# Performance work log

Hardware: AMD Instinct MI355X
Metric: run time of the kernel (lower is better)

## Reference

```python
import jax, jax.numpy as jnp
import numpy as np

NUM_HEADS = 32
HEAD_DIM = 128
HIDDEN = 4096
MAX_SEQ = 4096
B, S = 8, 16
POS = 2048


def setup_inputs() -> dict:
    key = jax.random.key(0)
    ks = jax.random.split(key, 7)
    sc = 1.0 / np.sqrt(HIDDEN)
    return {
        "h": jax.random.normal(ks[0], (B, S, HIDDEN), dtype=jnp.float32),
        "Wq": jax.random.normal(ks[1], (HIDDEN, HIDDEN), dtype=jnp.float32) * sc,
        "Wk": jax.random.normal(ks[2], (HIDDEN, HIDDEN), dtype=jnp.float32) * sc,
        "Wv": jax.random.normal(ks[3], (HIDDEN, HIDDEN), dtype=jnp.float32) * sc,
        "Wo": jax.random.normal(ks[4], (HIDDEN, HIDDEN), dtype=jnp.float32) * sc,
        "K_cache": jax.random.normal(ks[5], (B, NUM_HEADS, MAX_SEQ, HEAD_DIM), dtype=jnp.float32),
        "V_cache": jax.random.normal(ks[6], (B, NUM_HEADS, MAX_SEQ, HEAD_DIM), dtype=jnp.float32),
        "pos": POS,
    }


def reference(h, Wq, Wk, Wv, Wo, K_cache, V_cache, pos):
    b, s, _ = h.shape
    # QKV projections (Linear with weight [out, in], no bias): h @ W.T
    def proj(W):
        return (h @ W.T).reshape(b, s, NUM_HEADS, HEAD_DIM).transpose(0, 2, 1, 3)  # [B,H,S,hd]
    Q, K, V = proj(Wq), proj(Wk), proj(Wv)
    # write new K/V into cache at [pos : pos+S] (pos is a static Python int)
    K_cache = K_cache.at[:, :, pos:pos + s, :].set(K)
    V_cache = V_cache.at[:, :, pos:pos + s, :].set(V)
    K_all = K_cache[:, :, :pos + s, :]  # [B,H,T,hd], T = pos+S
    V_all = V_cache[:, :, :pos + s, :]
    scores = jnp.einsum('bhsd,bhtd->bhst', Q, K_all) / np.sqrt(HEAD_DIM)  # [B,H,S,T]
    if s > 1:
        # causal mask applied only to the freshly-written block of columns
        causal = jnp.triu(jnp.full((s, s), -jnp.inf, dtype=scores.dtype), k=1)
        scores = scores.at[:, :, :, pos:pos + s].add(causal)
    attn = jax.nn.softmax(scores, axis=-1)
    out = jnp.einsum('bhst,bhtd->bhsd', attn, V_all)  # [B,H,S,hd]
    out = out.transpose(0, 2, 1, 3).reshape(b, s, NUM_HEADS * HEAD_DIM)
    return out @ Wo.T
```

## Files before the change

kernel.cpp:

```cpp
#include <hip/hip_runtime.h>

typedef _Float16 f16;
typedef _Float16 f16x8 __attribute__((ext_vector_type(8)));
typedef _Float16 f16x2 __attribute__((ext_vector_type(2)));
typedef float f32x4 __attribute__((ext_vector_type(4)));
typedef float f32x2 __attribute__((ext_vector_type(2)));

#define MFMA16(a, b, c) __builtin_amdgcn_mfma_f32_16x16x32_f16(a, b, c, 0, 0, 0)

#define HID 4096
#define ROWS 128
#define SCL 0.12751743f

__device__ __forceinline__ f16x8 cvt8(float4 x, float4 y) {
    f16x8 v = {(f16)x.x, (f16)x.y, (f16)x.z, (f16)x.w,
               (f16)y.x, (f16)y.y, (f16)y.z, (f16)y.w};
    return v;
}

__device__ __forceinline__ int swz2(int row, int cb) {
    return row * 256 + (cb ^ ((row & 7) << 4));
}

__global__ void k_cvt(const float* __restrict__ src, f16* __restrict__ dst) {
    const int i = blockIdx.x * blockDim.x + threadIdx.x;
    const float4* s4 = (const float4*)src + (size_t)i * 2;
    float4 x = s4[0], y = s4[1];
    *((f16x8*)dst + i) = cvt8(x, y);
}

__global__ __launch_bounds__(256) void k_proj(
        const f16* __restrict__ hb,
        const float* __restrict__ Wq, const float* __restrict__ Wk,
        const float* __restrict__ Wv,
        f16* __restrict__ Qw, f16* __restrict__ Kw, f16* __restrict__ Vw) {
    const int mat = blockIdx.x >> 8;
    const int ct  = blockIdx.x & 255;
    const float* __restrict__ W = (mat == 0) ? Wq : (mat == 1) ? Wk : Wv;
    f16* __restrict__ Ob = (mat == 0) ? Qw : (mat == 1) ? Kw : Vw;
    const int c0 = ct * 16;

    __shared__ __align__(16) f16 sA[128 * 128];
    __shared__ __align__(16) f16 sB[16 * 128];

    const int tid = threadIdx.x;
    const int w = tid >> 6, l = tid & 63;
    const int rw = w * 32;
    const int ar = tid >> 4;
    const int ac = (tid & 15) * 8;

    f32x4 acc0 = {}, acc1 = {};

    for (int ks = 0; ks < 32; ++ks) {
        const int k0 = ks * 128;
        #pragma unroll
        for (int c = 0; c < 8; ++c) {
            const int row = c * 16 + ar;
            f16x8 v = *(const f16x8*)(hb + (size_t)row * HID + k0 + ac);
            *(f16x8*)((char*)sA + swz2(row, ac * 2)) = v;
        }
        {
            const float* wp = W + (size_t)(c0 + ar) * HID + k0 + ac;
            float4 x = *(const float4*)wp;
            float4 y = *(const float4*)(wp + 4);
            *(f16x8*)((char*)sB + swz2(ar, ac * 2)) = cvt8(x, y);
        }
        __syncthreads();
        #pragma unroll
        for (int kk = 0; kk < 4; ++kk) {
            const int cb = kk * 64 + (l >> 4) * 16;
            f16x8 a0 = *(const f16x8*)((char*)sA + swz2(rw + (l & 15), cb));
            f16x8 a1 = *(const f16x8*)((char*)sA + swz2(rw + 16 + (l & 15), cb));
            f16x8 b0 = *(const f16x8*)((char*)sB + swz2((l & 15), cb));
            acc0 = MFMA16(a0, b0, acc0);
            acc1 = MFMA16(a1, b0, acc1);
        }
        __syncthreads();
    }
    #pragma unroll
    for (int r = 0; r < 4; ++r) {
        const int col = c0 + (l & 15);
        Ob[(size_t)(rw + (l >> 4) * 4 + r) * HID + col]      = (f16)acc0[r];
        Ob[(size_t)(rw + 16 + (l >> 4) * 4 + r) * HID + col] = (f16)acc1[r];
    }
}

__global__ __launch_bounds__(1024) void k_attn(
        const f16* __restrict__ Qw, const f16* __restrict__ Kw,
        const f16* __restrict__ Vw,
        const float* __restrict__ Kc, const float* __restrict__ Vc,
        const int* __restrict__ posp, f16* __restrict__ Ow) {

    __shared__ __align__(16) char smem[131072 + 2048];

    const int bh = blockIdx.x;
    const int b = bh >> 5, hh = bh & 31;
    const int tid = threadIdx.x, w = tid >> 6, l = tid & 63;
    const int pos = *posp;
    const int ntiles = (pos + 16 + 31) >> 5;

    const float* Kb = Kc + (size_t)bh * (4096 * 128);
    const float* Vb = Vc + (size_t)bh * (4096 * 128);

    f16x8 qf[4];
    {
        const f16* qp = Qw + (size_t)(b * 16 + (l & 15)) * HID + hh * 128 + (l >> 4) * 8;
        #pragma unroll
        for (int kk = 0; kk < 4; ++kk) qf[kk] = *(const f16x8*)(qp + kk * 32);
    }

    f32x4 o[8] = {};
    float m[4], lsum[4];
    #pragma unroll
    for (int r = 0; r < 4; ++r) { m[r] = -3e38f; lsum[r] = 0.f; }

    f16* Pw = (f16*)smem + w * 640;

    for (int tau = w; tau < ntiles; tau += 16) {
        const int t0 = tau * 32;
        const bool pure = (t0 + 32 <= pos);
        f32x4 sa[2] = {};

        if (pure) {
            #pragma unroll
            for (int tn = 0; tn < 2; ++tn) {
                const float* kp = Kb + (size_t)(t0 + tn * 16 + (l & 15)) * 128 + (l >> 4) * 8;
                #pragma unroll
                for (int kk = 0; kk < 4; ++kk) {
                    float4 x = *(const float4*)(kp + kk * 32);
                    float4 y = *(const float4*)(kp + kk * 32 + 4);
                    sa[tn] = MFMA16(qf[kk], cvt8(x, y), sa[tn]);
                }
            }
        } else {
            #pragma unroll
            for (int tn = 0; tn < 2; ++tn) {
                const int trow = t0 + tn * 16 + (l & 15);
                f16x8 kf[4];
                if (trow < pos) {
                    const float* kp = Kb + (size_t)trow * 128 + (l >> 4) * 8;
                    #pragma unroll
                    for (int kk = 0; kk < 4; ++kk) {
                        float4 x = *(const float4*)(kp + kk * 32);
                        float4 y = *(const float4*)(kp + kk * 32 + 4);
                        kf[kk] = cvt8(x, y);
                    }
                } else {
                    const int tt = trow - pos;
                    const int rr = tt < 15 ? tt : 15;
                    const f16* kp = Kw + (size_t)(b * 16 + rr) * HID + hh * 128 + (l >> 4) * 8;
                    #pragma unroll
                    for (int kk = 0; kk < 4; ++kk) kf[kk] = *(const f16x8*)(kp + kk * 32);
                }
                #pragma unroll
                for (int kk = 0; kk < 4; ++kk) sa[tn] = MFMA16(qf[kk], kf[kk], sa[tn]);
            }
        }

        float sc[2][4];
        #pragma unroll
        for (int tn = 0; tn < 2; ++tn)
            #pragma unroll
            for (int r = 0; r < 4; ++r) sc[tn][r] = sa[tn][r] * SCL;
        if (!pure) {
            #pragma unroll
            for (int tn = 0; tn < 2; ++tn) {
                const int tg = t0 + tn * 16 + (l & 15);
                if (tg >= pos) {
                    const int tt = tg - pos;
                    #pragma unroll
                    for (int r = 0; r < 4; ++r) {
                        const int s_ = (l >> 4) * 4 + r;
                        if (tt > s_ || tt >= 16) sc[tn][r] = -3e38f;
                    }
                }
            }
        }

        float vmax[4];
        #pragma unroll
        for (int r = 0; r < 4; ++r) vmax[r] = fmaxf(sc[0][r], sc[1][r]);
        #pragma unroll
        for (int d = 1; d < 16; d <<= 1)
            #pragma unroll
            for (int r = 0; r < 4; ++r) vmax[r] = fmaxf(vmax[r], __shfl_xor(vmax[r], d));
        float p[2][4], rs[4], fac[4];
        #pragma unroll
        for (int r = 0; r < 4; ++r) {
            const float mn = fmaxf(m[r], vmax[r]);
            fac[r] = exp2f(m[r] - mn);
            m[r] = mn;
            p[0][r] = sc[0][r] < -1e29f ? 0.f : exp2f(sc[0][r] - mn);
            p[1][r] = sc[1][r] < -1e29f ? 0.f : exp2f(sc[1][r] - mn);
            rs[r] = p[0][r] + p[1][r];
            lsum[r] *= fac[r];
        }
        #pragma unroll
        for (int d = 1; d < 16; d <<= 1)
            #pragma unroll
            for (int r = 0; r < 4; ++r) rs[r] += __shfl_xor(rs[r], d);
        #pragma unroll
        for (int r = 0; r < 4; ++r) lsum[r] += rs[r];
        #pragma unroll
        for (int dt = 0; dt < 8; ++dt)
            #pragma unroll
            for (int r = 0; r < 4; ++r) o[dt][r] *= fac[r];

        #pragma unroll
        for (int r = 0; r < 4; ++r) {
            const int s_ = (l >> 4) * 4 + r;
            Pw[s_ * 40 + (l & 15)]      = (f16)p[0][r];
            Pw[s_ * 40 + 16 + (l & 15)] = (f16)p[1][r];
        }
        asm volatile("s_waitcnt lgkmcnt(0)" ::: "memory");
        f16x8 pa = *(const f16x8*)(Pw + (l & 15) * 40 + (l >> 4) * 8);

        if (pure) {
            const float* vp = Vb + (size_t)(t0 + (l >> 4) * 8) * 128 + (l & 15);
            #pragma unroll
            for (int dt = 0; dt < 8; ++dt) {
                f16x8 vf;
                #pragma unroll
                for (int j = 0; j < 8; ++j) vf[j] = (f16)vp[j * 128 + dt * 16];
                o[dt] = MFMA16(pa, vf, o[dt]);
            }
        } else {
            const int tb = t0 + (l >> 4) * 8;
            #pragma unroll
            for (int dt = 0; dt < 8; ++dt) {
                f16x8 vf;
                #pragma unroll
                for (int j = 0; j < 8; ++j) {
                    const int t = tb + j;
                    if (t < pos) {
                        vf[j] = (f16)Vb[(size_t)t * 128 + dt * 16 + (l & 15)];
                    } else {
                        const int rr = (t - pos < 15) ? (t - pos) : 15;
                        vf[j] = Vw[(size_t)(b * 16 + rr) * HID + hh * 128 + dt * 16 + (l & 15)];
                    }
                }
                o[dt] = MFMA16(pa, vf, o[dt]);
            }
        }
    }

    __syncthreads();
    float* Osh = (float*)smem;
    float* Msh = (float*)(smem + 131072);
    float* Lsh = Msh + 256;
    #pragma unroll
    for (int dt = 0; dt < 8; ++dt)
        #pragma unroll
        for (int r = 0; r < 4; ++r)
            Osh[w * 2048 + ((l >> 4) * 4 + r) * 128 + dt * 16 + (l & 15)] = o[dt][r];
    if ((l & 15) == 0) {
        #pragma unroll
        for (int r = 0; r < 4; ++r) {
            Msh[w * 16 + (l >> 4) * 4 + r] = m[r];
            Lsh[w * 16 + (l >> 4) * 4 + r] = lsum[r];
        }
    }
    __syncthreads();
    {
        const int s_ = tid >> 6;
        const int d_ = (tid & 63) * 2;
        float M = -3e38f;
        #pragma unroll
        for (int ww = 0; ww < 16; ++ww) M = fmaxf(M, Msh[ww * 16 + s_]);
        float L = 0.f, o0 = 0.f, o1 = 0.f;
        #pragma unroll
        for (int ww = 0; ww < 16; ++ww) {
            const float e = exp2f(Msh[ww * 16 + s_] - M);
            L += e * Lsh[ww * 16 + s_];
            f32x2 v = *(const f32x2*)(Osh + ww * 2048 + s_ * 128 + d_);
            o0 += e * v.x;
            o1 += e * v.y;
        }
        const float inv = 1.f / L;
        f16x2 res = {(f16)(o0 * inv), (f16)(o1 * inv)};
        *(f16x2*)(Ow + (size_t)(b * 16 + s_) * HID + hh * 128 + d_) = res;
    }
}

__global__ __launch_bounds__(256) void k_oproj(
        const f16* __restrict__ Oa, const float* __restrict__ Wo,
        float* __restrict__ out) {
    const int c0 = blockIdx.x * 16;

    __shared__ __align__(16) f16 sA[128 * 128];
    __shared__ __align__(16) f16 sB[16 * 128];

    const int tid = threadIdx.x;
    const int w = tid >> 6, l = tid & 63;
    const int rw = w * 32;
    const int ar = tid >> 4;
    const int ac = (tid & 15) * 8;

    f32x4 acc0 = {}, acc1 = {};

    for (int ks = 0; ks < 32; ++ks) {
        const int k0 = ks * 128;
        #pragma unroll
        for (int c = 0; c < 8; ++c) {
            const int row = c * 16 + ar;
            f16x8 v = *(const f16x8*)(Oa + (size_t)row * HID + k0 + ac);
            *(f16x8*)((char*)sA + swz2(row, ac * 2)) = v;
        }
        {
            const float* wp = Wo + (size_t)(c0 + ar) * HID + k0 + ac;
            float4 x = *(const float4*)wp;
            float4 y = *(const float4*)(wp + 4);
            *(f16x8*)((char*)sB + swz2(ar, ac * 2)) = cvt8(x, y);
        }
        __syncthreads();
        #pragma unroll
        for (int kk = 0; kk < 4; ++kk) {
            const int cb = kk * 64 + (l >> 4) * 16;
            f16x8 a0 = *(const f16x8*)((char*)sA + swz2(rw + (l & 15), cb));
            f16x8 a1 = *(const f16x8*)((char*)sA + swz2(rw + 16 + (l & 15), cb));
            f16x8 b0 = *(const f16x8*)((char*)sB + swz2((l & 15), cb));
            acc0 = MFMA16(a0, b0, acc0);
            acc1 = MFMA16(a1, b0, acc1);
        }
        __syncthreads();
    }
    #pragma unroll
    for (int r = 0; r < 4; ++r) {
        const int col = c0 + (l & 15);
        out[(size_t)(rw + (l >> 4) * 4 + r) * HID + col]      = acc0[r];
        out[(size_t)(rw + 16 + (l >> 4) * 4 + r) * HID + col] = acc1[r];
    }
}

extern "C" void kernel_launch(void* const* d_in, const int* in_sizes, int n_in,
                              void* d_out, int out_size, void* d_ws, size_t ws_size,
                              hipStream_t stream) {
    const float* h  = (const float*)d_in[0];
    const float* Wq = (const float*)d_in[1];
    const float* Wk = (const float*)d_in[2];
    const float* Wv = (const float*)d_in[3];
    const float* Wo = (const float*)d_in[4];
    const float* Kc = (const float*)d_in[5];
    const float* Vc = (const float*)d_in[6];
    const int* pos  = (const int*)d_in[7];
    float* out = (float*)d_out;

    f16* hws = (f16*)d_ws;
    f16* Qw  = hws + ROWS * HID;
    f16* Kw  = Qw + ROWS * HID;
    f16* Vw  = Kw + ROWS * HID;
    f16* Ow  = Vw + ROWS * HID;

    k_cvt<<<256, 256, 0, stream>>>(h, hws);
    k_proj<<<768, 256, 0, stream>>>(hws, Wq, Wk, Wv, Qw, Kw, Vw);
    k_attn<<<256, 1024, 0, stream>>>(Qw, Kw, Vw, Kc, Vc, pos, Ow);
    k_oproj<<<256, 256, 0, stream>>>(Ow, Wo, out);
}
```

Baseline: 241.3 us.

## Register-prefetch GEMM tiles and restructure attention into contiguous per-wave tile ranges

Both projection GEMMs now load the next K-slice of activations and weights into registers while the current slice is multiplied, so global loads overlap with MFMA work. The attention kernel drops from 16 to 8 waves per block. Each wave now processes a contiguous range of unmasked KV tiles with no masking branches, and V loads are issued earlier. A single wave handles the tail tiles that touch the new tokens, and the final reduction across waves uses wider vectors. This adds register pressure and a possible load imbalance from the tail wave, but cuts branching and lets more latency overlap.

```diff
diff --git a/kernel.cpp b/kernel.cpp
--- a/kernel.cpp
+++ b/kernel.cpp
@@ -2,6 +2,7 @@
 
 typedef _Float16 f16;
 typedef _Float16 f16x8 __attribute__((ext_vector_type(8)));
+typedef _Float16 f16x4 __attribute__((ext_vector_type(4)));
 typedef _Float16 f16x2 __attribute__((ext_vector_type(2)));
 typedef float f32x4 __attribute__((ext_vector_type(4)));
 typedef float f32x2 __attribute__((ext_vector_type(2)));
@@ -51,21 +52,30 @@
 
     f32x4 acc0 = {}, acc1 = {};
 
+    float4 wx, wy;
+    f16x8 hreg[8];
+    {
+        const float* wp = W + (size_t)(c0 + ar) * HID + ac;
+        wx = *(const float4*)wp; wy = *(const float4*)(wp + 4);
+        #pragma unroll
+        for (int c = 0; c < 8; ++c)
+            hreg[c] = *(const f16x8*)(hb + (size_t)(c * 16 + ar) * HID + ac);
+    }
+
     for (int ks = 0; ks < 32; ++ks) {
-        const int k0 = ks * 128;
-        #pragma unroll
-        for (int c = 0; c < 8; ++c) {
-            const int row = c * 16 + ar;
-            f16x8 v = *(const f16x8*)(hb + (size_t)row * HID + k0 + ac);
-            *(f16x8*)((char*)sA + swz2(row, ac * 2)) = v;
-        }
-        {
+        #pragma unroll
+        for (int c = 0; c < 8; ++c)
+            *(f16x8*)((char*)sA + swz2(c * 16 + ar, ac * 2)) = hreg[c];
+        *(f16x8*)((char*)sB + swz2(ar, ac * 2)) = cvt8(wx, wy);
+        __syncthreads();
+        if (ks < 31) {
+            const int k0 = (ks + 1) * 128;
             const float* wp = W + (size_t)(c0 + ar) * HID + k0 + ac;
-            float4 x = *(const float4*)wp;
-            float4 y = *(const float4*)(wp + 4);
-            *(f16x8*)((char*)sB + swz2(ar, ac * 2)) = cvt8(x, y);
-        }
-        __syncthreads();
+            wx = *(const float4*)wp; wy = *(const float4*)(wp + 4);
+            #pragma unroll
+            for (int c = 0; c < 8; ++c)
+                hreg[c] = *(const f16x8*)(hb + (size_t)(c * 16 + ar) * HID + k0 + ac);
+        }
         #pragma unroll
         for (int kk = 0; kk < 4; ++kk) {
             const int cb = kk * 64 + (l >> 4) * 16;
@@ -85,19 +95,19 @@
     }
 }
 
-__global__ __launch_bounds__(1024) void k_attn(
+__global__ __launch_bounds__(512) void k_attn(
         const f16* __restrict__ Qw, const f16* __restrict__ Kw,
         const f16* __restrict__ Vw,
         const float* __restrict__ Kc, const float* __restrict__ Vc,
         const int* __restrict__ posp, f16* __restrict__ Ow) {
 
-    __shared__ __align__(16) char smem[131072 + 2048];
+    __shared__ __align__(16) char smem[65536 + 1024];
 
     const int bh = blockIdx.x;
     const int b = bh >> 5, hh = bh & 31;
     const int tid = threadIdx.x, w = tid >> 6, l = tid & 63;
     const int pos = *posp;
-    const int ntiles = (pos + 16 + 31) >> 5;
+    const int npure = pos >> 5;
 
     const float* Kb = Kc + (size_t)bh * (4096 * 128);
     const float* Vb = Vc + (size_t)bh * (4096 * 128);
@@ -116,25 +126,92 @@
 
     f16* Pw = (f16*)smem + w * 640;
 
-    for (int tau = w; tau < ntiles; tau += 16) {
-        const int t0 = tau * 32;
-        const bool pure = (t0 + 32 <= pos);
+    const int start = (w * npure) >> 3;
+    const int end   = ((w + 1) * npure) >> 3;
+    for (int tau = start; tau < end; ++tau) {
+        const int t0 = tau << 5;
+
+        f16x8 kf[2][4];
+        #pragma unroll
+        for (int tn = 0; tn < 2; ++tn) {
+            const float* kp = Kb + (size_t)(t0 + tn * 16 + (l & 15)) * 128 + (l >> 4) * 8;
+            #pragma unroll
+            for (int kk = 0; kk < 4; ++kk) {
+                float4 x = *(const float4*)(kp + kk * 32);
+                float4 y = *(const float4*)(kp + kk * 32 + 4);
+                kf[tn][kk] = cvt8(x, y);
+            }
+        }
         f32x4 sa[2] = {};
-
-        if (pure) {
+        #pragma unroll
+        for (int tn = 0; tn < 2; ++tn)
+            #pragma unroll
+            for (int kk = 0; kk < 4; ++kk) sa[tn] = MFMA16(qf[kk], kf[tn][kk], sa[tn]);
+
+        f16x8 vf[8];
+        {
+            const float* vp = Vb + (size_t)(t0 + (l >> 4) * 8) * 128 + (l & 15);
+            #pragma unroll
+            for (int dt = 0; dt < 8; ++dt)
+                #pragma unroll
+                for (int j = 0; j < 8; ++j) vf[dt][j] = (f16)vp[j * 128 + dt * 16];
+        }
+
+        float sc[2][4];
+        #pragma unroll
+        for (int tn = 0; tn < 2; ++tn)
+            #pragma unroll
+            for (int r = 0; r < 4; ++r) sc[tn][r] = sa[tn][r] * SCL;
+        float vmax[4];
+        #pragma unroll
+        for (int r = 0; r < 4; ++r) vmax[r] = fmaxf(sc[0][r], sc[1][r]);
+        #pragma unroll
+        for (int d = 1; d < 16; d <<= 1)
+            #pragma unroll
+            for (int r = 0; r < 4; ++r) vmax[r] = fmaxf(vmax[r], __shfl_xor(vmax[r], d));
+        float p[2][4], rs[4], fac[4];
+        #pragma unroll
+        for (int r = 0; r < 4; ++r) {
+            const float mn = fmaxf(m[r], vmax[r]);
+            fac[r] = exp2f(m[r] - mn);
+            m[r] = mn;
+            p[0][r] = exp2f(sc[0][r] - mn);
+            p[1][r] = exp2f(sc[1][r] - mn);
+            rs[r] = p[0][r] + p[1][r];
+            lsum[r] *= fac[r];
+        }
+        #pragma unroll
+        for (int d = 1; d < 16; d <<= 1)
+            #pragma unroll
+            for (int r = 0; r < 4; ++r) rs[r] += __shfl_xor(rs[r], d);
+        #pragma unroll
+        for (int r = 0; r < 4; ++r) lsum[r] += rs[r];
+        #pragma unroll
+        for (int dt = 0; dt < 8; ++dt)
+            #pragma unroll
+            for (int r = 0; r < 4; ++r) o[dt][r] *= fac[r];
+
+        #pragma unroll
+        for (int r = 0; r < 4; ++r) {
+            const int s_ = (l >> 4) * 4 + r;
+            Pw[s_ * 40 + (l & 15)]      = (f16)p[0][r];
+            Pw[s_ * 40 + 16 + (l & 15)] = (f16)p[1][r];
+        }
+        asm volatile("s_waitcnt lgkmcnt(0)" ::: "memory");
+        f16x8 pa = *(const f16x8*)(Pw + (l & 15) * 40 + (l >> 4) * 8);
+
+        #pragma unroll
+        for (int dt = 0; dt < 8; ++dt) o[dt] = MFMA16(pa, vf[dt], o[dt]);
+    }
+
+    if (w == 7) {
+        for (int t0 = npure << 5; t0 < pos + 16; t0 += 32) {
+            f32x4 sa[2] = {};
+            bool tnv[2];
             #pragma unroll
             for (int tn = 0; tn < 2; ++tn) {
-                const float* kp = Kb + (size_t)(t0 + tn * 16 + (l & 15)) * 128 + (l >> 4) * 8;
-                #pragma unroll
-                for (int kk = 0; kk < 4; ++kk) {
-                    float4 x = *(const float4*)(kp + kk * 32);
-                    float4 y = *(const float4*)(kp + kk * 32 + 4);
-                    sa[tn] = MFMA16(qf[kk], cvt8(x, y), sa[tn]);
-                }
-            }
-        } else {
-            #pragma unroll
-            for (int tn = 0; tn < 2; ++tn) {
+                tnv[tn] = (t0 + tn * 16 < pos + 16);
+                if (!tnv[tn]) continue;
                 const int trow = t0 + tn * 16 + (l & 15);
                 f16x8 kf[4];
                 if (trow < pos) {
@@ -155,76 +232,62 @@
                 #pragma unroll
                 for (int kk = 0; kk < 4; ++kk) sa[tn] = MFMA16(qf[kk], kf[kk], sa[tn]);
             }
-        }
-
-        float sc[2][4];
-        #pragma unroll
-        for (int tn = 0; tn < 2; ++tn)
-            #pragma unroll
-            for (int r = 0; r < 4; ++r) sc[tn][r] = sa[tn][r] * SCL;
-        if (!pure) {
+
+            float sc[2][4];
             #pragma unroll
             for (int tn = 0; tn < 2; ++tn) {
                 const int tg = t0 + tn * 16 + (l & 15);
-                if (tg >= pos) {
-                    const int tt = tg - pos;
-                    #pragma unroll
-                    for (int r = 0; r < 4; ++r) {
+                #pragma unroll
+                for (int r = 0; r < 4; ++r) {
+                    if (!tnv[tn]) { sc[tn][r] = -3e38f; continue; }
+                    float v = sa[tn][r] * SCL;
+                    if (tg >= pos) {
+                        const int tt = tg - pos;
                         const int s_ = (l >> 4) * 4 + r;
-                        if (tt > s_ || tt >= 16) sc[tn][r] = -3e38f;
+                        if (tt > s_ || tt >= 16) v = -3e38f;
                     }
+                    sc[tn][r] = v;
                 }
             }
-        }
-
-        float vmax[4];
-        #pragma unroll
-        for (int r = 0; r < 4; ++r) vmax[r] = fmaxf(sc[0][r], sc[1][r]);
-        #pragma unroll
-        for (int d = 1; d < 16; d <<= 1)
-            #pragma unroll
-            for (int r = 0; r < 4; ++r) vmax[r] = fmaxf(vmax[r], __shfl_xor(vmax[r], d));
-        float p[2][4], rs[4], fac[4];
-        #pragma unroll
-        for (int r = 0; r < 4; ++r) {
-            const float mn = fmaxf(m[r], vmax[r]);
-            fac[r] = exp2f(m[r] - mn);
-            m[r] = mn;
-            p[0][r] = sc[0][r] < -1e29f ? 0.f : exp2f(sc[0][r] - mn);
-            p[1][r] = sc[1][r] < -1e29f ? 0.f : exp2f(sc[1][r] - mn);
-            rs[r] = p[0][r] + p[1][r];
-            lsum[r] *= fac[r];
-        }
-        #pragma unroll
-        for (int d = 1; d < 16; d <<= 1)
-            #pragma unroll
-            for (int r = 0; r < 4; ++r) rs[r] += __shfl_xor(rs[r], d);
-        #pragma unroll
-        for (int r = 0; r < 4; ++r) lsum[r] += rs[r];
-        #pragma unroll
-        for (int dt = 0; dt < 8; ++dt)
-            #pragma unroll
-            for (int r = 0; r < 4; ++r) o[dt][r] *= fac[r];
-
-        #pragma unroll
-        for (int r = 0; r < 4; ++r) {
-            const int s_ = (l >> 4) * 4 + r;
-            Pw[s_ * 40 + (l & 15)]      = (f16)p[0][r];
-            Pw[s_ * 40 + 16 + (l & 15)] = (f16)p[1][r];
-        }
-        asm volatile("s_waitcnt lgkmcnt(0)" ::: "memory");
-        f16x8 pa = *(const f16x8*)(Pw + (l & 15) * 40 + (l >> 4) * 8);
-
-        if (pure) {
-            const float* vp = Vb + (size_t)(t0 + (l >> 4) * 8) * 128 + (l & 15);
-            #pragma unroll
-            for (int dt = 0; dt < 8; ++dt) {
-                f16x8 vf;
-                #pragma unroll
-                for (int j = 0; j < 8; ++j) vf[j] = (f16)vp[j * 128 + dt * 16];
-                o[dt] = MFMA16(pa, vf, o[dt]);
-            }
-        } else {
+
+            float vmax[4];
+            #pragma unroll
+            for (int r = 0; r < 4; ++r) vmax[r] = fmaxf(sc[0][r], sc[1][r]);
+            #pragma unroll
+            for (int d = 1; d < 16; d <<= 1)
+                #pragma unroll
+                for (int r = 0; r < 4; ++r) vmax[r] = fmaxf(vmax[r], __shfl_xor(vmax[r], d));
+            float p[2][4], rs[4], fac[4];
+            #pragma unroll
+            for (int r = 0; r < 4; ++r) {
+                const float mn = fmaxf(m[r], vmax[r]);
+                fac[r] = exp2f(m[r] - mn);
+                m[r] = mn;
+                p[0][r] = sc[0][r] < -1e29f ? 0.f : exp2f(sc[0][r] - mn);
+                p[1][r] = sc[1][r] < -1e29f ? 0.f : exp2f(sc[1][r] - mn);
+                rs[r] = p[0][r] + p[1][r];
+                lsum[r] *= fac[r];
+            }
+            #pragma unroll
+            for (int d = 1; d < 16; d <<= 1)
+                #pragma unroll
+                for (int r = 0; r < 4; ++r) rs[r] += __shfl_xor(rs[r], d);
+            #pragma unroll
+            for (int r = 0; r < 4; ++r) lsum[r] += rs[r];
+            #pragma unroll
+            for (int dt = 0; dt < 8; ++dt)
+                #pragma unroll
+                for (int r = 0; r < 4; ++r) o[dt][r] *= fac[r];
+
+            #pragma unroll
+            for (int r = 0; r < 4; ++r) {
+                const int s_ = (l >> 4) * 4 + r;
+                Pw[s_ * 40 + (l & 15)]      = (f16)p[0][r];
+                Pw[s_ * 40 + 16 + (l & 15)] = (f16)p[1][r];
+            }
+            asm volatile("s_waitcnt lgkmcnt(0)" ::: "memory");
+            f16x8 pa = *(const f16x8*)(Pw + (l & 15) * 40 + (l >> 4) * 8);
+
             const int tb = t0 + (l >> 4) * 8;
             #pragma unroll
             for (int dt = 0; dt < 8; ++dt) {
@@ -246,8 +309,8 @@
 
     __syncthreads();
     float* Osh = (float*)smem;
-    float* Msh = (float*)(smem + 131072);
-    float* Lsh = Msh + 256;
+    float* Msh = (float*)(smem + 65536);
+    float* Lsh = Msh + 128;
     #pragma unroll
     for (int dt = 0; dt < 8; ++dt)
         #pragma unroll
@@ -262,23 +325,25 @@
     }
     __syncthreads();
     {
-        const int s_ = tid >> 6;
-        const int d_ = (tid & 63) * 2;
+        const int s_ = tid >> 5;
+        const int d_ = (tid & 31) * 4;
         float M = -3e38f;
         #pragma unroll
-        for (int ww = 0; ww < 16; ++ww) M = fmaxf(M, Msh[ww * 16 + s_]);
-        float L = 0.f, o0 = 0.f, o1 = 0.f;
-        #pragma unroll
-        for (int ww = 0; ww < 16; ++ww) {
+        for (int ww = 0; ww < 8; ++ww) M = fmaxf(M, Msh[ww * 16 + s_]);
+        float L = 0.f;
+        f32x4 oa = {};
+        #pragma unroll
+        for (int ww = 0; ww < 8; ++ww) {
             const float e = exp2f(Msh[ww * 16 + s_] - M);
             L += e * Lsh[ww * 16 + s_];
-            f32x2 v = *(const f32x2*)(Osh + ww * 2048 + s_ * 128 + d_);
-            o0 += e * v.x;
-            o1 += e * v.y;
+            f32x4 v = *(const f32x4*)(Osh + ww * 2048 + s_ * 128 + d_);
+            #pragma unroll
+            for (int r = 0; r < 4; ++r) oa[r] += e * v[r];
         }
         const float inv = 1.f / L;
-        f16x2 res = {(f16)(o0 * inv), (f16)(o1 * inv)};
-        *(f16x2*)(Ow + (size_t)(b * 16 + s_) * HID + hh * 128 + d_) = res;
+        f16x4 res = {(f16)(oa[0] * inv), (f16)(oa[1] * inv),
+                     (f16)(oa[2] * inv), (f16)(oa[3] * inv)};
+        *(f16x4*)(Ow + (size_t)(b * 16 + s_) * HID + hh * 128 + d_) = res;
     }
 }
 
@@ -298,21 +363,30 @@
 
     f32x4 acc0 = {}, acc1 = {};
 
+    float4 wx, wy;
+    f16x8 hreg[8];
+    {
+        const float* wp = Wo + (size_t)(c0 + ar) * HID + ac;
+        wx = *(const float4*)wp; wy = *(const float4*)(wp + 4);
+        #pragma unroll
+        for (int c = 0; c < 8; ++c)
+            hreg[c] = *(const f16x8*)(Oa + (size_t)(c * 16 + ar) * HID + ac);
+    }
+
     for (int ks = 0; ks < 32; ++ks) {
-        const int k0 = ks * 128;
-        #pragma unroll
-        for (int c = 0; c < 8; ++c) {
-            const int row = c * 16 + ar;
-            f16x8 v = *(const f16x8*)(Oa + (size_t)row * HID + k0 + ac);
-            *(f16x8*)((char*)sA + swz2(row, ac * 2)) = v;
-        }
-        {
+        #pragma unroll
+        for (int c = 0; c < 8; ++c)
+            *(f16x8*)((char*)sA + swz2(c * 16 + ar, ac * 2)) = hreg[c];
+        *(f16x8*)((char*)sB + swz2(ar, ac * 2)) = cvt8(wx, wy);
+        __syncthreads();
+        if (ks < 31) {
+            const int k0 = (ks + 1) * 128;
             const float* wp = Wo + (size_t)(c0 + ar) * HID + k0 + ac;
-            float4 x = *(const float4*)wp;
-            float4 y = *(const float4*)(wp + 4);
-            *(f16x8*)((char*)sB + swz2(ar, ac * 2)) = cvt8(x, y);
-        }
-        __syncthreads();
+            wx = *(const float4*)wp; wy = *(const float4*)(wp + 4);
+            #pragma unroll
+            for (int c = 0; c < 8; ++c)
+                hreg[c] = *(const f16x8*)(Oa + (size_t)(c * 16 + ar) * HID + k0 + ac);
+        }
         #pragma unroll
         for (int kk = 0; kk < 4; ++kk) {
             const int cb = kk * 64 + (l >> 4) * 16;
@@ -353,6 +427,6 @@
 
     k_cvt<<<256, 256, 0, stream>>>(h, hws);
     k_proj<<<768, 256, 0, stream>>>(hws, Wq, Wk, Wv, Qw, Kw, Vw);
-    k_attn<<<256, 1024, 0, stream>>>(Qw, Kw, Vw, Kc, Vc, pos, Ow);
+    k_attn<<<256, 512, 0, stream>>>(Qw, Kw, Vw, Kc, Vc, pos, Ow);
     k_oproj<<<256, 256, 0, stream>>>(Ow, Wo, out);
 }
```

New measurement: 205.6 us. 14.8% less time.
